# Kernel optimization log

Hardware: AMD Instinct MI355X
Metric: run time of the kernel (lower is better)

Reference implementation:

```python
import jax, jax.numpy as jnp
import numpy as np

H = 512
TEMPERATURE = 1.0


def setup_inputs() -> dict:
    key = jax.random.key(0)
    ks = jax.random.split(key, 9)
    B, Q, S = 4, 64, 1024
    scale = 1.0 / np.sqrt(H)
    return {
        "query": jax.random.normal(ks[0], (B, Q, H), jnp.float32),
        "key_": jax.random.normal(ks[1], (B, S, H), jnp.float32),
        "value": jax.random.normal(ks[2], (B, S, H), jnp.float32),
        "Wq": jax.random.normal(ks[3], (H, H), jnp.float32) * scale,
        "bq": jax.random.normal(ks[4], (H,), jnp.float32) * 0.01,
        "Wk": jax.random.normal(ks[5], (H, H), jnp.float32) * scale,
        "bk": jax.random.normal(ks[6], (H,), jnp.float32) * 0.01,
        "we": jax.random.normal(ks[7], (H,), jnp.float32) * scale,
        "be": jax.random.normal(ks[8], (), jnp.float32) * 0.01,
    }


def reference(query, key_, value, Wq, bq, Wk, bk, we, be):
    # query: [B,Q,H], key_/value: [B,S,H]
    qp = jnp.einsum("bqd,dh->bqh", query, Wq) + bq          # [B,Q,H]
    kp = jnp.einsum("bsd,dh->bsh", key_, Wk) + bk           # [B,S,H]
    attn_sum = jnp.tanh(qp[:, :, None, :] + kp[:, None, :, :])  # [B,Q,S,H]
    scores = (jnp.einsum("bqsh,h->bqs", attn_sum, we) + be) / TEMPERATURE
    weights = jax.nn.softmax(scores, axis=-1)               # [B,Q,S]
    context = jnp.einsum("bqs,bsh->bqh", weights, value)    # [B,Q,H]
    return context, weights
```

## Files before the change

kernel.cpp:

```cpp
#include <hip/hip_runtime.h>


constexpr int kB = 4;
constexpr int kQ = 64;
constexpr int kS = 1024;
constexpr int kH = 512;

typedef short bf16x8 __attribute__((ext_vector_type(8)));
typedef float f32x4 __attribute__((ext_vector_type(4)));

__device__ __forceinline__ unsigned bf16rtn_bits(float x) {
  unsigned u = __float_as_uint(x);
  u += 0x7FFFu + ((u >> 16) & 1u);
  return u;
}

__global__ __launch_bounds__(256) void convert_w(
    const float* __restrict__ Wk, const float* __restrict__ Wq,
    unsigned short* __restrict__ Bhi, unsigned short* __restrict__ Blo) {
  const int gid = blockIdx.x * 256 + threadIdx.x;
  const int c = gid & 63;
  const int g = (gid >> 6) & 3;
  const int kt = (gid >> 8) & 15;
  const int ct = (gid >> 12) & 7;
  const int mat = gid >> 15;
  const float* W = mat ? Wq : Wk;
  const float* src = W + (size_t)(kt * 32 + g * 8) * kH + ct * 64 + c;
  bf16x8 hv, lv;
#pragma unroll
  for (int j = 0; j < 8; j++) {
    float x = src[(size_t)j * kH];
    unsigned u = bf16rtn_bits(x);
    float hf = __uint_as_float(u & 0xFFFF0000u);
    unsigned v = bf16rtn_bits(x - hf);
    hv[j] = (short)(u >> 16);
    lv[j] = (short)(v >> 16);
  }
  *(bf16x8*)(Bhi + (size_t)gid * 8) = hv;
  *(bf16x8*)(Blo + (size_t)gid * 8) = lv;
}

__global__ __launch_bounds__(256) void proj_mfma(
    const float* __restrict__ key_, const float* __restrict__ query,
    const unsigned short* __restrict__ Bhi, const unsigned short* __restrict__ Blo,
    const float* __restrict__ bk, const float* __restrict__ bq,
    float* __restrict__ Ek, float* __restrict__ Eq) {
  __shared__ __align__(16) unsigned short AhiL[2][2048];
  __shared__ __align__(16) unsigned short AloL[2][2048];
  __shared__ __align__(16) unsigned short BhiL[2][2048];
  __shared__ __align__(16) unsigned short BloL[2][2048];

  const int ct = blockIdx.x;
  int rt = blockIdx.y;
  const float* X;
  const float* bias;
  float* Y;
  int mat;
  if (rt < 64) {
    X = key_ + (size_t)rt * 64 * kH; bias = bk; Y = Ek + (size_t)rt * 64 * kH; mat = 0;
  } else {
    rt -= 64;
    X = query + (size_t)rt * 64 * kH; bias = bq; Y = Eq + (size_t)rt * 64 * kH; mat = 1;
  }

  const int t = threadIdx.x;
  const int ar = t & 63, ag = t >> 6;
  const float* aptr = X + (size_t)ar * kH + ag * 8;
  const unsigned short* bht = Bhi + ((size_t)(mat * 8 + ct) * 16) * 2048 + t * 8;
  const unsigned short* blt = Blo + ((size_t)(mat * 8 + ct) * 16) * 2048 + t * 8;

  float4 pa0, pa1;
  uint4 pbh, pbl;
  auto gload = [&](int kt2) {
    const float* p = aptr + kt2 * 32;
    pa0 = *(const float4*)p;
    pa1 = *(const float4*)(p + 4);
    pbh = *(const uint4*)(bht + (size_t)kt2 * 2048);
    pbl = *(const uint4*)(blt + (size_t)kt2 * 2048);
  };
  auto cwrite = [&](int buf) {
    bf16x8 hv, lv;
#define CVT1(x, e)                                          \
  {                                                         \
    unsigned u = bf16rtn_bits(x);                           \
    float hf = __uint_as_float(u & 0xFFFF0000u);            \
    unsigned v = bf16rtn_bits((x) - hf);                    \
    hv[e] = (short)(u >> 16);                               \
    lv[e] = (short)(v >> 16);                               \
  }
    CVT1(pa0.x, 0) CVT1(pa0.y, 1) CVT1(pa0.z, 2) CVT1(pa0.w, 3)
    CVT1(pa1.x, 4) CVT1(pa1.y, 5) CVT1(pa1.z, 6) CVT1(pa1.w, 7)
#undef CVT1
    *(bf16x8*)&AhiL[buf][t * 8] = hv;
    *(bf16x8*)&AloL[buf][t * 8] = lv;
    *(uint4*)&BhiL[buf][t * 8] = pbh;
    *(uint4*)&BloL[buf][t * 8] = pbl;
  };

  const int l = t & 63, lg = l >> 4, lr = l & 15;
  const int wv = t >> 6, wm = wv >> 1, wn = wv & 1;
  const int oa0 = (lg * 64 + (2 * wm) * 16 + lr) * 8;
  const int ob0 = (lg * 64 + (2 * wn) * 16 + lr) * 8;

  f32x4 acc00 = {0.f, 0.f, 0.f, 0.f};
  f32x4 acc01 = acc00, acc10 = acc00, acc11 = acc00;

  gload(0);
  cwrite(0);
  __syncthreads();

#pragma unroll 2
  for (int kt2 = 0; kt2 < 16; kt2++) {
    if (kt2 < 15) gload(kt2 + 1);

    const unsigned short* Ah = AhiL[kt2 & 1];
    const unsigned short* Al = AloL[kt2 & 1];
    const unsigned short* Bh = BhiL[kt2 & 1];
    const unsigned short* Bl = BloL[kt2 & 1];
    bf16x8 ah0 = *(const bf16x8*)(Ah + oa0);
    bf16x8 ah1 = *(const bf16x8*)(Ah + oa0 + 128);
    bf16x8 al0 = *(const bf16x8*)(Al + oa0);
    bf16x8 al1 = *(const bf16x8*)(Al + oa0 + 128);
    bf16x8 bh0 = *(const bf16x8*)(Bh + ob0);
    bf16x8 bh1 = *(const bf16x8*)(Bh + ob0 + 128);
    bf16x8 bl0 = *(const bf16x8*)(Bl + ob0);
    bf16x8 bl1 = *(const bf16x8*)(Bl + ob0 + 128);

    acc00 = __builtin_amdgcn_mfma_f32_16x16x32_bf16(ah0, bh0, acc00, 0, 0, 0);
    acc01 = __builtin_amdgcn_mfma_f32_16x16x32_bf16(ah0, bh1, acc01, 0, 0, 0);
    acc10 = __builtin_amdgcn_mfma_f32_16x16x32_bf16(ah1, bh0, acc10, 0, 0, 0);
    acc11 = __builtin_amdgcn_mfma_f32_16x16x32_bf16(ah1, bh1, acc11, 0, 0, 0);
    acc00 = __builtin_amdgcn_mfma_f32_16x16x32_bf16(al0, bh0, acc00, 0, 0, 0);
    acc01 = __builtin_amdgcn_mfma_f32_16x16x32_bf16(al0, bh1, acc01, 0, 0, 0);
    acc10 = __builtin_amdgcn_mfma_f32_16x16x32_bf16(al1, bh0, acc10, 0, 0, 0);
    acc11 = __builtin_amdgcn_mfma_f32_16x16x32_bf16(al1, bh1, acc11, 0, 0, 0);
    acc00 = __builtin_amdgcn_mfma_f32_16x16x32_bf16(ah0, bl0, acc00, 0, 0, 0);
    acc01 = __builtin_amdgcn_mfma_f32_16x16x32_bf16(ah0, bl1, acc01, 0, 0, 0);
    acc10 = __builtin_amdgcn_mfma_f32_16x16x32_bf16(ah1, bl0, acc10, 0, 0, 0);
    acc11 = __builtin_amdgcn_mfma_f32_16x16x32_bf16(ah1, bl1, acc11, 0, 0, 0);

    if (kt2 < 15) {
      cwrite((kt2 + 1) & 1);
      __syncthreads();
    }
  }

  const int n0 = ct * 64;
  const int col0 = n0 + (2 * wn) * 16 + lr;
  const float b0 = bias[col0];
  const float b1 = bias[col0 + 16];
  const int row0 = (2 * wm) * 16 + lg * 4;
#pragma unroll
  for (int jj = 0; jj < 4; jj++) {
    float* y = Y + (size_t)(row0 + jj) * kH;
    y[col0]      = __expf(2.f * (acc00[jj] + b0));
    y[col0 + 16] = __expf(2.f * (acc01[jj] + b1));
    float* y2 = y + (size_t)16 * kH;
    y2[col0]      = __expf(2.f * (acc10[jj] + b0));
    y2[col0 + 16] = __expf(2.f * (acc11[jj] + b1));
  }
}

__global__ __launch_bounds__(256) void score_kernel(
    const float* __restrict__ Eq, const float* __restrict__ Ek,
    const float* __restrict__ we, float* __restrict__ sout) {
  __shared__ __align__(16) float EkL[2][64 * 64];
  __shared__ __align__(16) float EqL[8 * 512];
  __shared__ __align__(16) float wL[512];

  const int qt = blockIdx.x, st = blockIdx.y, b = blockIdx.z;
  const int t = threadIdx.x, wv = t >> 6, lane = t & 63;
  const int s0 = st * 64;
  const int q0g = b * kQ + qt * 8;
  const int qA = wv * 2;

  const float4* we4 = (const float4*)(we + lane * 8);
  float4 u0 = we4[0], u1 = we4[1];
  float wsum = u0.x + u0.y + u0.z + u0.w + u1.x + u1.y + u1.z + u1.w;
#pragma unroll
  for (int off = 32; off; off >>= 1) wsum += __shfl_xor(wsum, off);

  if (t < 128) {
    float4 w = ((const float4*)we)[t];
    w.x *= -2.f; w.y *= -2.f; w.z *= -2.f; w.w *= -2.f;
    ((float4*)wL)[t] = w;
  }
  {
    const float4* src = (const float4*)(Eq + (size_t)q0g * kH);
#pragma unroll
    for (int i = 0; i < 4; i++) {
      int idx = t + 256 * i;
      ((float4*)EqL)[idx] = src[idx];
    }
  }

  const int er = t >> 4;
  const int ej = t & 15;
  const float* ekg = Ek + (size_t)(b * kS + s0 + er) * kH + ej * 4;
  float4 pk[4];
  auto gload = [&](int c) {
#pragma unroll
    for (int i = 0; i < 4; i++)
      pk[i] = *(const float4*)(ekg + (size_t)(16 * i) * kH + c * 64);
  };
  auto lwrite = [&](int buf) {
#pragma unroll
    for (int i = 0; i < 4; i++) {
      const int row = er + 16 * i;
      *(float4*)(&EkL[buf][row * 64 + ((ej ^ (row & 15)) << 2)]) = pk[i];
    }
  };

  gload(0);
  lwrite(0);
  __syncthreads();

  float accA = 0.f, accB = 0.f;
  const int sw = lane & 15;
  const float* eqa = EqL + (qA + 0) * 512;
  const float* eqb = EqL + (qA + 1) * 512;

  for (int c = 0; c < 8; c++) {
    if (c < 7) gload(c + 1);
    const float* ekb = &EkL[c & 1][lane * 64];
    const float* wc = wL + c * 64;
    const float* ea = eqa + c * 64;
    const float* eb = eqb + c * 64;
#pragma unroll 4
    for (int g = 0; g < 16; g++) {
      float4 ek = *(const float4*)(ekb + ((g ^ sw) << 2));
      float4 w = *(const float4*)(wc + g * 4);
      float4 qa = *(const float4*)(ea + g * 4);
      float4 qb = *(const float4*)(eb + g * 4);
      {
        float a1 = fmaf(qa.x, ek.x, 1.f), b1 = fmaf(qa.y, ek.y, 1.f);
        float n1 = fmaf(w.y, a1, w.x * b1);
        accA = fmaf(n1, __builtin_amdgcn_rcpf(a1 * b1), accA);
        float a2 = fmaf(qa.z, ek.z, 1.f), b2 = fmaf(qa.w, ek.w, 1.f);
        float n2 = fmaf(w.w, a2, w.z * b2);
        accA = fmaf(n2, __builtin_amdgcn_rcpf(a2 * b2), accA);
      }
      {
        float a1 = fmaf(qb.x, ek.x, 1.f), b1 = fmaf(qb.y, ek.y, 1.f);
        float n1 = fmaf(w.y, a1, w.x * b1);
        accB = fmaf(n1, __builtin_amdgcn_rcpf(a1 * b1), accB);
        float a2 = fmaf(qb.z, ek.z, 1.f), b2 = fmaf(qb.w, ek.w, 1.f);
        float n2 = fmaf(w.w, a2, w.z * b2);
        accB = fmaf(n2, __builtin_amdgcn_rcpf(a2 * b2), accB);
      }
    }
    if (c < 7) {
      __syncthreads();
      lwrite((c + 1) & 1);
      __syncthreads();
    }
  }

  sout[(size_t)(q0g + qA + 0) * kS + s0 + lane] = accA + wsum;
  sout[(size_t)(q0g + qA + 1) * kS + s0 + lane] = accB + wsum;
}

__global__ __launch_bounds__(256) void softmax_kernel(float* __restrict__ wout) {
  __shared__ float redm[4];
  __shared__ float reds[4];
  const int row = blockIdx.x;
  const int t = threadIdx.x, wave = t >> 6, lane = t & 63;
  float4* rp = (float4*)(wout + (size_t)row * kS);
  float4 v = rp[t];

  float m = fmaxf(fmaxf(v.x, v.y), fmaxf(v.z, v.w));
#pragma unroll
  for (int off = 32; off; off >>= 1) m = fmaxf(m, __shfl_xor(m, off));
  if (lane == 0) redm[wave] = m;
  __syncthreads();
  m = fmaxf(fmaxf(redm[0], redm[1]), fmaxf(redm[2], redm[3]));

  float4 e;
  e.x = __expf(v.x - m); e.y = __expf(v.y - m);
  e.z = __expf(v.z - m); e.w = __expf(v.w - m);
  float sum = e.x + e.y + e.z + e.w;
#pragma unroll
  for (int off = 32; off; off >>= 1) sum += __shfl_xor(sum, off);
  if (lane == 0) reds[wave] = sum;
  __syncthreads();
  sum = reds[0] + reds[1] + reds[2] + reds[3];
  float inv = 1.f / sum;
  e.x *= inv; e.y *= inv; e.z *= inv; e.w *= inv;
  rp[t] = e;
}

__global__ __launch_bounds__(256) void context_kernel(
    const float* __restrict__ wout, const float* __restrict__ value,
    float* __restrict__ part) {
  __shared__ __align__(16) float wt[128][16];
  const int bx = blockIdx.x;
  const int sc = bx & 7, qc = (bx >> 3) & 3, hc = (bx >> 5) & 1, b = bx >> 6;
  const int t = threadIdx.x;
  const int s0 = sc * 128, q0 = qc * 16;

  {
    const int q_l = t & 15;
    const int sseg = (t >> 4) * 8;
    const float4* p4 =
        (const float4*)(wout + (size_t)(b * kQ + q0 + q_l) * kS + s0 + sseg);
    float4 u0 = p4[0], u1 = p4[1];
    wt[sseg + 0][q_l] = u0.x; wt[sseg + 1][q_l] = u0.y;
    wt[sseg + 2][q_l] = u0.z; wt[sseg + 3][q_l] = u0.w;
    wt[sseg + 4][q_l] = u1.x; wt[sseg + 5][q_l] = u1.y;
    wt[sseg + 6][q_l] = u1.z; wt[sseg + 7][q_l] = u1.w;
  }
  __syncthreads();

  const int h = hc * 256 + t;
  const float* vb = value + ((size_t)b * kS + s0) * kH + h;
  float acc[16];
#pragma unroll
  for (int i = 0; i < 16; i++) acc[i] = 0.f;

#pragma unroll 4
  for (int s = 0; s < 128; s++) {
    float v = vb[(size_t)s * kH];
    const float4* wrow = (const float4*)&wt[s][0];
    float4 a0 = wrow[0], a1 = wrow[1], a2 = wrow[2], a3 = wrow[3];
    acc[0]  = fmaf(a0.x, v, acc[0]);  acc[1]  = fmaf(a0.y, v, acc[1]);
    acc[2]  = fmaf(a0.z, v, acc[2]);  acc[3]  = fmaf(a0.w, v, acc[3]);
    acc[4]  = fmaf(a1.x, v, acc[4]);  acc[5]  = fmaf(a1.y, v, acc[5]);
    acc[6]  = fmaf(a1.z, v, acc[6]);  acc[7]  = fmaf(a1.w, v, acc[7]);
    acc[8]  = fmaf(a2.x, v, acc[8]);  acc[9]  = fmaf(a2.y, v, acc[9]);
    acc[10] = fmaf(a2.z, v, acc[10]); acc[11] = fmaf(a2.w, v, acc[11]);
    acc[12] = fmaf(a3.x, v, acc[12]); acc[13] = fmaf(a3.y, v, acc[13]);
    acc[14] = fmaf(a3.z, v, acc[14]); acc[15] = fmaf(a3.w, v, acc[15]);
  }

  float* pp = part + (size_t)sc * kB * kQ * kH;
#pragma unroll
  for (int i = 0; i < 16; i++)
    pp[(size_t)(b * kQ + q0 + i) * kH + h] = acc[i];
}

__global__ __launch_bounds__(256) void reduce_kernel(
    const float* __restrict__ part, float* __restrict__ ctx) {
  const int i = blockIdx.x * 256 + threadIdx.x;
  float4 a = {0, 0, 0, 0};
#pragma unroll
  for (int p = 0; p < 8; p++) {
    float4 v = ((const float4*)(part + (size_t)p * kB * kQ * kH))[i];
    a.x += v.x; a.y += v.y; a.z += v.z; a.w += v.w;
  }
  ((float4*)ctx)[i] = a;
}

extern "C" void kernel_launch(void* const* d_in, const int* in_sizes, int n_in,
                              void* d_out, int out_size, void* d_ws,
                              size_t ws_size, hipStream_t stream) {
  const float* query = (const float*)d_in[0];
  const float* key_  = (const float*)d_in[1];
  const float* value = (const float*)d_in[2];
  const float* Wq    = (const float*)d_in[3];
  const float* bq    = (const float*)d_in[4];
  const float* Wk    = (const float*)d_in[5];
  const float* bk    = (const float*)d_in[6];
  const float* we    = (const float*)d_in[7];

  float* ctx  = (float*)d_out;
  float* wout = (float*)d_out + (size_t)kB * kQ * kH;

  float* Eq   = (float*)d_ws;
  float* Ek   = Eq + (size_t)kB * kQ * kH;
  float* part = Ek;
  unsigned short* Bhi =
      (unsigned short*)((char*)d_ws + (size_t)(kB * kQ * kH + kB * kS * kH) * 4);
  unsigned short* Blo = Bhi + (size_t)2 * 8 * 16 * 256 * 8;

  convert_w<<<256, 256, 0, stream>>>(Wk, Wq, Bhi, Blo);
  proj_mfma<<<dim3(8, 68), 256, 0, stream>>>(key_, query, Bhi, Blo, bk, bq, Ek, Eq);
  score_kernel<<<dim3(8, 16, 4), 256, 0, stream>>>(Eq, Ek, we, wout);
  softmax_kernel<<<kB * kQ, 256, 0, stream>>>(wout);
  context_kernel<<<256, 256, 0, stream>>>(wout, value, part);
  reduce_kernel<<<kB * kQ * kH / 4 / 256, 256, 0, stream>>>(part, ctx);
}
```

Before: 150.1 us.

## Pre-split activations to bf16 hi/lo, enlarge projection tiles, read score operands directly

Adds a convert_x kernel that splits key and query rows into bf16 hi/lo halves once, in a tile-friendly layout. proj_mfma then streams these pre-converted tiles and uses 512 threads with 128-row tiles, which halves the number of times the weight tiles are reloaded and removes per-block conversion work. The score kernel no longer stages Eq and the scaled weight vector in shared memory; it reads them straight from global memory, relying on the cache, and folds the -2 factor into the final fma. The cost is an extra kernel launch and an extra write and read of the converted activations through memory.

```diff
diff --git a/kernel.cpp b/kernel.cpp
--- a/kernel.cpp
+++ b/kernel.cpp
@@ -40,76 +40,93 @@
   *(bf16x8*)(Blo + (size_t)gid * 8) = lv;
 }
 
-__global__ __launch_bounds__(256) void proj_mfma(
+__global__ __launch_bounds__(256) void convert_x(
     const float* __restrict__ key_, const float* __restrict__ query,
+    unsigned short* __restrict__ Xhi, unsigned short* __restrict__ Xlo) {
+  __shared__ __align__(16) unsigned short LHi[128 * 40];
+  __shared__ __align__(16) unsigned short LLo[128 * 40];
+  const int kt = blockIdx.x;
+  const int rt = blockIdx.y;
+  const float* X = (rt < 32) ? (key_ + (size_t)rt * 128 * kH)
+                             : (query + (size_t)(rt - 32) * 128 * kH);
+  const int t = threadIdx.x;
+  const int r = t >> 1, c0 = (t & 1) * 16;
+  const float* src = X + (size_t)r * kH + kt * 32 + c0;
+  bf16x8 hv0, hv1, lv0, lv1;
+#pragma unroll
+  for (int i = 0; i < 16; i++) {
+    float x = src[i];
+    unsigned u = bf16rtn_bits(x);
+    float hf = __uint_as_float(u & 0xFFFF0000u);
+    unsigned v = bf16rtn_bits(x - hf);
+    if (i < 8) { hv0[i] = (short)(u >> 16); lv0[i] = (short)(v >> 16); }
+    else       { hv1[i - 8] = (short)(u >> 16); lv1[i - 8] = (short)(v >> 16); }
+  }
+  *(bf16x8*)&LHi[r * 40 + c0] = hv0;
+  *(bf16x8*)&LHi[r * 40 + c0 + 8] = hv1;
+  *(bf16x8*)&LLo[r * 40 + c0] = lv0;
+  *(bf16x8*)&LLo[r * 40 + c0 + 8] = lv1;
+  __syncthreads();
+  const size_t obase = (size_t)(rt * 16 + kt) * 512 * 8;
+#pragma unroll
+  for (int p = 0; p < 2; p++) {
+    const int s = t + p * 256;
+    const int rr = s & 127, g = s >> 7;
+    *(uint4*)(Xhi + obase + (size_t)s * 8) = *(const uint4*)&LHi[rr * 40 + g * 8];
+    *(uint4*)(Xlo + obase + (size_t)s * 8) = *(const uint4*)&LLo[rr * 40 + g * 8];
+  }
+}
+
+__global__ __launch_bounds__(512) void proj_mfma(
+    const unsigned short* __restrict__ Xhi, const unsigned short* __restrict__ Xlo,
     const unsigned short* __restrict__ Bhi, const unsigned short* __restrict__ Blo,
     const float* __restrict__ bk, const float* __restrict__ bq,
     float* __restrict__ Ek, float* __restrict__ Eq) {
-  __shared__ __align__(16) unsigned short AhiL[2][2048];
-  __shared__ __align__(16) unsigned short AloL[2][2048];
+  __shared__ __align__(16) unsigned short AhiL[2][4096];
+  __shared__ __align__(16) unsigned short AloL[2][4096];
   __shared__ __align__(16) unsigned short BhiL[2][2048];
   __shared__ __align__(16) unsigned short BloL[2][2048];
 
   const int ct = blockIdx.x;
-  int rt = blockIdx.y;
-  const float* X;
-  const float* bias;
-  float* Y;
-  int mat;
-  if (rt < 64) {
-    X = key_ + (size_t)rt * 64 * kH; bias = bk; Y = Ek + (size_t)rt * 64 * kH; mat = 0;
-  } else {
-    rt -= 64;
-    X = query + (size_t)rt * 64 * kH; bias = bq; Y = Eq + (size_t)rt * 64 * kH; mat = 1;
-  }
+  const int rt = blockIdx.y;
+  const int mat = (rt >= 32) ? 1 : 0;
+  const float* bias = mat ? bq : bk;
+  float* Y = mat ? (Eq + (size_t)(rt - 32) * 128 * kH)
+                 : (Ek + (size_t)rt * 128 * kH);
 
   const int t = threadIdx.x;
-  const int ar = t & 63, ag = t >> 6;
-  const float* aptr = X + (size_t)ar * kH + ag * 8;
-  const unsigned short* bht = Bhi + ((size_t)(mat * 8 + ct) * 16) * 2048 + t * 8;
-  const unsigned short* blt = Blo + ((size_t)(mat * 8 + ct) * 16) * 2048 + t * 8;
-
-  float4 pa0, pa1;
-  uint4 pbh, pbl;
+  const unsigned short* ah_src = Xhi + ((size_t)(rt * 16) * 512 + t) * 8;
+  const unsigned short* al_src = Xlo + ((size_t)(rt * 16) * 512 + t) * 8;
+  const int bslot = t & 255;
+  const unsigned short* b_src =
+      ((t < 256) ? Bhi : Blo) + ((size_t)((mat * 8 + ct) * 16) * 256 + bslot) * 8;
+
+  uint4 pah, pal, pb;
   auto gload = [&](int kt2) {
-    const float* p = aptr + kt2 * 32;
-    pa0 = *(const float4*)p;
-    pa1 = *(const float4*)(p + 4);
-    pbh = *(const uint4*)(bht + (size_t)kt2 * 2048);
-    pbl = *(const uint4*)(blt + (size_t)kt2 * 2048);
+    pah = *(const uint4*)(ah_src + (size_t)kt2 * 512 * 8);
+    pal = *(const uint4*)(al_src + (size_t)kt2 * 512 * 8);
+    pb = *(const uint4*)(b_src + (size_t)kt2 * 256 * 8);
   };
-  auto cwrite = [&](int buf) {
-    bf16x8 hv, lv;
-#define CVT1(x, e)                                          \
-  {                                                         \
-    unsigned u = bf16rtn_bits(x);                           \
-    float hf = __uint_as_float(u & 0xFFFF0000u);            \
-    unsigned v = bf16rtn_bits((x) - hf);                    \
-    hv[e] = (short)(u >> 16);                               \
-    lv[e] = (short)(v >> 16);                               \
-  }
-    CVT1(pa0.x, 0) CVT1(pa0.y, 1) CVT1(pa0.z, 2) CVT1(pa0.w, 3)
-    CVT1(pa1.x, 4) CVT1(pa1.y, 5) CVT1(pa1.z, 6) CVT1(pa1.w, 7)
-#undef CVT1
-    *(bf16x8*)&AhiL[buf][t * 8] = hv;
-    *(bf16x8*)&AloL[buf][t * 8] = lv;
-    *(uint4*)&BhiL[buf][t * 8] = pbh;
-    *(uint4*)&BloL[buf][t * 8] = pbl;
+  auto lwrite = [&](int buf) {
+    *(uint4*)&AhiL[buf][t * 8] = pah;
+    *(uint4*)&AloL[buf][t * 8] = pal;
+    if (t < 256) *(uint4*)&BhiL[buf][bslot * 8] = pb;
+    else         *(uint4*)&BloL[buf][bslot * 8] = pb;
   };
 
   const int l = t & 63, lg = l >> 4, lr = l & 15;
-  const int wv = t >> 6, wm = wv >> 1, wn = wv & 1;
-  const int oa0 = (lg * 64 + (2 * wm) * 16 + lr) * 8;
-  const int ob0 = (lg * 64 + (2 * wn) * 16 + lr) * 8;
-
-  f32x4 acc00 = {0.f, 0.f, 0.f, 0.f};
-  f32x4 acc01 = acc00, acc10 = acc00, acc11 = acc00;
+  const int wv = t >> 6, wm = wv & 3, wn = wv >> 2;
+
+  f32x4 acc[2][2];
+#pragma unroll
+  for (int m = 0; m < 2; m++)
+#pragma unroll
+    for (int n = 0; n < 2; n++) acc[m][n] = {0.f, 0.f, 0.f, 0.f};
 
   gload(0);
-  cwrite(0);
-  __syncthreads();
-
-#pragma unroll 2
+  lwrite(0);
+  __syncthreads();
+
   for (int kt2 = 0; kt2 < 16; kt2++) {
     if (kt2 < 15) gload(kt2 + 1);
 
@@ -117,47 +134,47 @@
     const unsigned short* Al = AloL[kt2 & 1];
     const unsigned short* Bh = BhiL[kt2 & 1];
     const unsigned short* Bl = BloL[kt2 & 1];
-    bf16x8 ah0 = *(const bf16x8*)(Ah + oa0);
-    bf16x8 ah1 = *(const bf16x8*)(Ah + oa0 + 128);
-    bf16x8 al0 = *(const bf16x8*)(Al + oa0);
-    bf16x8 al1 = *(const bf16x8*)(Al + oa0 + 128);
-    bf16x8 bh0 = *(const bf16x8*)(Bh + ob0);
-    bf16x8 bh1 = *(const bf16x8*)(Bh + ob0 + 128);
-    bf16x8 bl0 = *(const bf16x8*)(Bl + ob0);
-    bf16x8 bl1 = *(const bf16x8*)(Bl + ob0 + 128);
-
-    acc00 = __builtin_amdgcn_mfma_f32_16x16x32_bf16(ah0, bh0, acc00, 0, 0, 0);
-    acc01 = __builtin_amdgcn_mfma_f32_16x16x32_bf16(ah0, bh1, acc01, 0, 0, 0);
-    acc10 = __builtin_amdgcn_mfma_f32_16x16x32_bf16(ah1, bh0, acc10, 0, 0, 0);
-    acc11 = __builtin_amdgcn_mfma_f32_16x16x32_bf16(ah1, bh1, acc11, 0, 0, 0);
-    acc00 = __builtin_amdgcn_mfma_f32_16x16x32_bf16(al0, bh0, acc00, 0, 0, 0);
-    acc01 = __builtin_amdgcn_mfma_f32_16x16x32_bf16(al0, bh1, acc01, 0, 0, 0);
-    acc10 = __builtin_amdgcn_mfma_f32_16x16x32_bf16(al1, bh0, acc10, 0, 0, 0);
-    acc11 = __builtin_amdgcn_mfma_f32_16x16x32_bf16(al1, bh1, acc11, 0, 0, 0);
-    acc00 = __builtin_amdgcn_mfma_f32_16x16x32_bf16(ah0, bl0, acc00, 0, 0, 0);
-    acc01 = __builtin_amdgcn_mfma_f32_16x16x32_bf16(ah0, bl1, acc01, 0, 0, 0);
-    acc10 = __builtin_amdgcn_mfma_f32_16x16x32_bf16(ah1, bl0, acc10, 0, 0, 0);
-    acc11 = __builtin_amdgcn_mfma_f32_16x16x32_bf16(ah1, bl1, acc11, 0, 0, 0);
+    bf16x8 ah[2], al[2], bh[2], bl[2];
+#pragma unroll
+    for (int m = 0; m < 2; m++) {
+      const int off = (lg * 128 + wm * 32 + m * 16 + lr) * 8;
+      ah[m] = *(const bf16x8*)(Ah + off);
+      al[m] = *(const bf16x8*)(Al + off);
+    }
+#pragma unroll
+    for (int n = 0; n < 2; n++) {
+      const int off = (lg * 64 + wn * 32 + n * 16 + lr) * 8;
+      bh[n] = *(const bf16x8*)(Bh + off);
+      bl[n] = *(const bf16x8*)(Bl + off);
+    }
+#pragma unroll
+    for (int m = 0; m < 2; m++)
+#pragma unroll
+      for (int n = 0; n < 2; n++) {
+        acc[m][n] = __builtin_amdgcn_mfma_f32_16x16x32_bf16(ah[m], bh[n], acc[m][n], 0, 0, 0);
+        acc[m][n] = __builtin_amdgcn_mfma_f32_16x16x32_bf16(al[m], bh[n], acc[m][n], 0, 0, 0);
+        acc[m][n] = __builtin_amdgcn_mfma_f32_16x16x32_bf16(ah[m], bl[n], acc[m][n], 0, 0, 0);
+      }
 
     if (kt2 < 15) {
-      cwrite((kt2 + 1) & 1);
       __syncthreads();
-    }
-  }
-
-  const int n0 = ct * 64;
-  const int col0 = n0 + (2 * wn) * 16 + lr;
+      lwrite((kt2 + 1) & 1);
+      __syncthreads();
+    }
+  }
+
+  const int col0 = ct * 64 + wn * 32 + lr;
   const float b0 = bias[col0];
   const float b1 = bias[col0 + 16];
-  const int row0 = (2 * wm) * 16 + lg * 4;
-#pragma unroll
-  for (int jj = 0; jj < 4; jj++) {
-    float* y = Y + (size_t)(row0 + jj) * kH;
-    y[col0]      = __expf(2.f * (acc00[jj] + b0));
-    y[col0 + 16] = __expf(2.f * (acc01[jj] + b1));
-    float* y2 = y + (size_t)16 * kH;
-    y2[col0]      = __expf(2.f * (acc10[jj] + b0));
-    y2[col0 + 16] = __expf(2.f * (acc11[jj] + b1));
+#pragma unroll
+  for (int m = 0; m < 2; m++) {
+    const int row0 = wm * 32 + m * 16 + lg * 4;
+#pragma unroll
+    for (int jj = 0; jj < 4; jj++) {
+      float* y = Y + (size_t)(row0 + jj) * kH;
+      y[col0]      = __expf(2.f * (acc[m][0][jj] + b0));
+      y[col0 + 16] = __expf(2.f * (acc[m][1][jj] + b1));
+    }
   }
 }
 
@@ -165,34 +182,24 @@
     const float* __restrict__ Eq, const float* __restrict__ Ek,
     const float* __restrict__ we, float* __restrict__ sout) {
   __shared__ __align__(16) float EkL[2][64 * 64];
-  __shared__ __align__(16) float EqL[8 * 512];
-  __shared__ __align__(16) float wL[512];
 
   const int qt = blockIdx.x, st = blockIdx.y, b = blockIdx.z;
-  const int t = threadIdx.x, wv = t >> 6, lane = t & 63;
+  const int t = threadIdx.x, lane = t & 63;
+  const int wvu = __builtin_amdgcn_readfirstlane(t >> 6);
   const int s0 = st * 64;
   const int q0g = b * kQ + qt * 8;
-  const int qA = wv * 2;
-
-  const float4* we4 = (const float4*)(we + lane * 8);
-  float4 u0 = we4[0], u1 = we4[1];
+  const int qA = wvu * 2;
+
+  const float4* we4 = (const float4*)we;
+  {
+  }
+  float4 u0 = we4[lane * 2], u1 = we4[lane * 2 + 1];
   float wsum = u0.x + u0.y + u0.z + u0.w + u1.x + u1.y + u1.z + u1.w;
 #pragma unroll
   for (int off = 32; off; off >>= 1) wsum += __shfl_xor(wsum, off);
 
-  if (t < 128) {
-    float4 w = ((const float4*)we)[t];
-    w.x *= -2.f; w.y *= -2.f; w.z *= -2.f; w.w *= -2.f;
-    ((float4*)wL)[t] = w;
-  }
-  {
-    const float4* src = (const float4*)(Eq + (size_t)q0g * kH);
-#pragma unroll
-    for (int i = 0; i < 4; i++) {
-      int idx = t + 256 * i;
-      ((float4*)EqL)[idx] = src[idx];
-    }
-  }
+  const float4* qa4 = (const float4*)(Eq + (size_t)(q0g + qA) * kH);
+  const float4* qb4 = (const float4*)(Eq + (size_t)(q0g + qA + 1) * kH);
 
   const int er = t >> 4;
   const int ej = t & 15;
@@ -217,21 +224,16 @@
 
   float accA = 0.f, accB = 0.f;
   const int sw = lane & 15;
-  const float* eqa = EqL + (qA + 0) * 512;
-  const float* eqb = EqL + (qA + 1) * 512;
 
   for (int c = 0; c < 8; c++) {
     if (c < 7) gload(c + 1);
     const float* ekb = &EkL[c & 1][lane * 64];
-    const float* wc = wL + c * 64;
-    const float* ea = eqa + c * 64;
-    const float* eb = eqb + c * 64;
 #pragma unroll 4
     for (int g = 0; g < 16; g++) {
       float4 ek = *(const float4*)(ekb + ((g ^ sw) << 2));
-      float4 w = *(const float4*)(wc + g * 4);
-      float4 qa = *(const float4*)(ea + g * 4);
-      float4 qb = *(const float4*)(eb + g * 4);
+      float4 w = we4[c * 16 + g];
+      float4 qa = qa4[c * 16 + g];
+      float4 qb = qb4[c * 16 + g];
       {
         float a1 = fmaf(qa.x, ek.x, 1.f), b1 = fmaf(qa.y, ek.y, 1.f);
         float n1 = fmaf(w.y, a1, w.x * b1);
@@ -256,8 +258,8 @@
     }
   }
 
-  sout[(size_t)(q0g + qA + 0) * kS + s0 + lane] = accA + wsum;
-  sout[(size_t)(q0g + qA + 1) * kS + s0 + lane] = accB + wsum;
+  sout[(size_t)(q0g + qA + 0) * kS + s0 + lane] = fmaf(-2.f, accA, wsum);
+  sout[(size_t)(q0g + qA + 1) * kS + s0 + lane] = fmaf(-2.f, accB, wsum);
 }
 
 __global__ __launch_bounds__(256) void softmax_kernel(float* __restrict__ wout) {
@@ -371,9 +373,12 @@
   unsigned short* Bhi =
       (unsigned short*)((char*)d_ws + (size_t)(kB * kQ * kH + kB * kS * kH) * 4);
   unsigned short* Blo = Bhi + (size_t)2 * 8 * 16 * 256 * 8;
+  unsigned short* Xhi = Blo + (size_t)2 * 8 * 16 * 256 * 8;
+  unsigned short* Xlo = Xhi + (size_t)34 * 16 * 512 * 8;
 
   convert_w<<<256, 256, 0, stream>>>(Wk, Wq, Bhi, Blo);
-  proj_mfma<<<dim3(8, 68), 256, 0, stream>>>(key_, query, Bhi, Blo, bk, bq, Ek, Eq);
+  convert_x<<<dim3(16, 34), 256, 0, stream>>>(key_, query, Xhi, Xlo);
+  proj_mfma<<<dim3(8, 34), 512, 0, stream>>>(Xhi, Xlo, Bhi, Blo, bk, bq, Ek, Eq);
   score_kernel<<<dim3(8, 16, 4), 256, 0, stream>>>(Eq, Ek, we, wout);
   softmax_kernel<<<kB * kQ, 256, 0, stream>>>(wout);
   context_kernel<<<256, 256, 0, stream>>>(wout, value, part);
```

Result: slower. 154.4 us (+2.9%).
